# Kernel tuning notes

Measured on AMD Instinct MI355X. Metric: run time of the kernel, lower is better.

Reference implementation:

```python
import jax, jax.numpy as jnp
import numpy as np
from jax import lax

NEG = -1e30  # log-space 'zero' (avoid -inf for numerical safety)
EPS = 1e-7   # keras.backend.epsilon(), added before log in ctc_batch_cost


def _ctc_loss(y_pred, y_true):
    """CTC negative log-likelihood, full input/label lengths, blank = C-1.

    y_pred: [B, T, C] probabilities (post-softmax, as keras ctc_batch_cost expects)
    y_true: [B, L] int labels in [0, C-2]
    returns [B, 1] loss per example (matches keras ctc_batch_cost output shape)
    """
    B, T, C = y_pred.shape
    L = y_true.shape[1]
    S = 2 * L + 1
    blank = C - 1

    logp = jnp.log(y_pred + EPS)  # [B, T, C]

    # Extended label sequence: blank, l1, blank, l2, ..., lL, blank
    ext = jnp.full((B, S), blank, dtype=y_true.dtype)
    ext = ext.at[:, 1::2].set(y_true)  # [B, S]

    # s-2 skip transition allowed iff ext[s] != blank and ext[s] != ext[s-2]
    allow = jnp.concatenate(
        [jnp.zeros((B, 2), dtype=bool),
         (ext[:, 2:] != blank) & (ext[:, 2:] != ext[:, :-2])], axis=1)  # [B, S]

    # Gather log-probs of extended labels per time step: [T, B, S]
    logp_t = jnp.transpose(logp, (1, 0, 2))  # [T, B, C]
    idx = jnp.broadcast_to(ext[None, :, :], (T, B, S))
    lp_ext = jnp.take_along_axis(logp_t, idx, axis=2)  # [T, B, S]

    # alpha init at t=0: only s=0 (blank) and s=1 (first label) reachable
    alpha0 = jnp.full((B, S), NEG, dtype=logp.dtype)
    alpha0 = alpha0.at[:, 0].set(lp_ext[0, :, 0])
    alpha0 = alpha0.at[:, 1].set(lp_ext[0, :, 1])

    neg1 = jnp.full((B, 1), NEG, dtype=logp.dtype)
    neg2 = jnp.full((B, 2), NEG, dtype=logp.dtype)

    def step(alpha, lp):
        a1 = jnp.concatenate([neg1, alpha[:, :-1]], axis=1)
        a2 = jnp.concatenate([neg2, alpha[:, :-2]], axis=1)
        a = jnp.logaddexp(alpha, a1)
        a = jnp.logaddexp(a, jnp.where(allow, a2, NEG))
        return a + lp, None

    alphaT, _ = lax.scan(step, alpha0, lp_ext[1:])  # sequential over T-1 steps

    loss = -jnp.logaddexp(alphaT[:, S - 1], alphaT[:, S - 2])  # [B]
    return loss[:, None]


def setup_inputs() -> dict:
    key = jax.random.key(0)
    k1, k2 = jax.random.split(key)
    B, T, C, L = 512, 512, 128, 64
    logits = jax.random.normal(k1, (B, T, C), dtype=jnp.float32)
    y_pred = jax.nn.softmax(logits, axis=-1)  # ctc_batch_cost expects probabilities
    y_true = jax.random.randint(k2, (B, L), 0, C - 1)  # labels in [0, C-2]; blank=C-1
    return {"y_true": y_true, "y_pred": y_pred}


def reference(y_true, y_pred):
    return _ctc_loss(y_pred, y_true)
```

## Files before the change

kernel.cpp:

```cpp
#include <hip/hip_runtime.h>
#include <hip/hip_bf16.h>


typedef unsigned int u32;
typedef unsigned long long u64;

constexpr int B = 512, T = 512, C = 128, L = 64;
constexpr int NCHUNK = T / 8;
constexpr float EPS = 1e-7f;
constexpr float LN2 = 0.69314718055994530942f;

__device__ __forceinline__ u32 rne16(u32 b) {
    return (b + 0x7FFFu + ((b >> 16) & 1u)) >> 16;
}
__device__ __forceinline__ double dpp64_shr1(double x) {
    union { double d; u32 u[2]; } in, out;
    in.d = x;
    out.u[0] = (u32)__builtin_amdgcn_update_dpp(0, (int)in.u[0], 0x138, 0xF, 0xF, false);
    out.u[1] = (u32)__builtin_amdgcn_update_dpp(0, (int)in.u[1], 0x138, 0xF, 0xF, false);
    return out.d;
}
template <int CTRL>
__device__ __forceinline__ u32 dpp_maxu_step(u32 m) {
    u32 t = (u32)__builtin_amdgcn_update_dpp(0, (int)m, CTRL, 0xF, 0xF, false);
    return m > t ? m : t;
}
__device__ __forceinline__ double exp2_exact(int e) {
    union { double d; u64 u; } s; s.u = (u64)(1023 + e) << 52; return s.d;
}

__global__ __launch_bounds__(512)
void ctc_fused(const int* __restrict__ y_true,
               const float* __restrict__ y_pred,
               float* __restrict__ out) {
    __shared__ uint4 sG[NCHUNK * 65];

    const int b    = blockIdx.x;
    const int wave = threadIdx.x >> 6;
    const int lane = threadIdx.x & 63;

    const int lab  = y_true[b * L + lane];
    const int perm = (lab >> 1) << 2;
    const bool sel_hi = (lab & 1);

    {
        const u64* __restrict__ base =
            (const u64*)(y_pred + (size_t)b * T * C) + lane;
        const int c0 = wave * 8;

        u64 buf[2][8];
#pragma unroll
        for (int j = 0; j < 8; ++j)
            buf[0][j] = __builtin_nontemporal_load(base + (c0 * 8 + j) * 64);

#pragma unroll
        for (int i = 0; i < 8; ++i) {
            const int c = c0 + i;
            if (i + 1 < 8) {
#pragma unroll
                for (int j = 0; j < 8; ++j)
                    buf[(i + 1) & 1][j] =
                        __builtin_nontemporal_load(base + ((c + 1) * 8 + j) * 64);
            }
            const u64* row = buf[i & 1];

            u32 gl[8], gb[8];
#pragma unroll
            for (int j = 0; j < 8; ++j) {
                const int lo = (int)(u32)row[j];
                const int hi = (int)(u32)(row[j] >> 32);
                const int vx = __builtin_amdgcn_ds_bpermute(perm, lo);
                const int vy = __builtin_amdgcn_ds_bpermute(perm, hi);
                gl[j] = __float_as_uint(__int_as_float(sel_hi ? vy : vx) + EPS);
                gb[j] = __float_as_uint(__int_as_float(__shfl(hi, 63)) + EPS);
            }
            u32 wl[4], wb[4];
#pragma unroll
            for (int q = 0; q < 4; ++q) {
                wl[q] = rne16(gl[2 * q]) | (rne16(gl[2 * q + 1]) << 16);
                wb[q] = rne16(gb[2 * q]) | (rne16(gb[2 * q + 1]) << 16);
            }
            sG[c * 65 + lane] = make_uint4(wl[0], wl[1], wl[2], wl[3]);
            if (lane == 0)
                sG[c * 65 + 64] = make_uint4(wb[0], wb[1], wb[2], wb[3]);
        }
    }
    __syncthreads();
    if (threadIdx.x >= 64) return;

    const int lab_prev = __shfl_up(lab, 1);
    const bool allow1 = (lane >= 1) && (lab != lab_prev);

    uint4 so[4], sb[4];
#pragma unroll
    for (int c = 0; c < 4; ++c) {
        so[c] = sG[c * 65 + lane];
        sb[c] = sG[c * 65 + 64];
    }

    double d0 = (lane == 0) ? 1.0 : 0.0;
    double d1 = 0.0;
    double d2 = 0.0;
    int Ce = 0;

#pragma unroll 4
    for (int c = 0; c < NCHUNK; ++c) {
        const int slot = c & 3;
        const uint4 uo = so[slot];
        const uint4 ub = sb[slot];
        const int nc = c + 4;
        if (nc < NCHUNK) {
            so[slot] = sG[nc * 65 + lane];
            sb[slot] = sG[nc * 65 + 64];
        }

        const u32* ow = (const u32*)&uo;
        const u32* bw = (const u32*)&ub;
#pragma unroll
        for (int j = 0; j < 8; ++j) {
            const u32 wo = ow[j >> 1], wb = bw[j >> 1];
            const float fl = __uint_as_float((j & 1) ? (wo & 0xFFFF0000u) : (wo << 16));
            const float fb = __uint_as_float((j & 1) ? (wb & 0xFFFF0000u) : (wb << 16));
            const double Pl = (double)fl, Pb = (double)fb;
            const double p0  = dpp64_shr1(d1);
            const double s01 = d0 + d1;
            const double sel = allow1 ? p0 : 0.0;
            const double nd0 = (d0 + p0) * Pb;
            const double nd2 = (d2 + d1) * Pb;
            const double nd1 = (s01 + sel) * Pl;
            d0 = nd0; d1 = nd1; d2 = nd2;
        }

        if ((c & 3) == 3) {
            u32 h0 = (u32)__double2hiint(d0);
            u32 h1 = (u32)__double2hiint(d1);
            u32 m = h0 > h1 ? h0 : h1;
            m = dpp_maxu_step<0x111>(m);
            m = dpp_maxu_step<0x112>(m);
            m = dpp_maxu_step<0x114>(m);
            m = dpp_maxu_step<0x118>(m);
            m = dpp_maxu_step<0x142>(m);
            m = dpp_maxu_step<0x143>(m);
            const u32 M = (u32)__builtin_amdgcn_readlane((int)m, 63);
            const int e = (int)((M >> 20) & 0x7FFu) - 1023;
            const double s = exp2_exact(-e);
            d0 *= s; d1 *= s; d2 *= s;
            Ce += e;
        }
    }

    if (lane == 63) {
        const double sum = d1 + d2;
        const int ee = ((__double2hiint(sum) >> 20) & 0x7FF) - 1023;
        const float mant = (float)(sum * exp2_exact(-ee));
        out[b] = -((float)(Ce + ee) + __log2f(mant)) * LN2;
    }
}

extern "C" void kernel_launch(void* const* d_in, const int* in_sizes, int n_in,
                              void* d_out, int out_size, void* d_ws, size_t ws_size,
                              hipStream_t stream) {
    const int*   y_true = (const int*)d_in[0];
    const float* y_pred = (const float*)d_in[1];
    float*       out    = (float*)d_out;
    ctc_fused<<<dim3(B), dim3(512), 0, stream>>>(y_true, y_pred, out);
}
```

Measured before the change: 205.1 us.

## Overlap CTC alpha recursion with gather stage using per-chunk LDS ready flags

Replaces the block-wide barrier between the gather/convert stage and the sequential alpha recursion with per-chunk ready flags in shared memory. Waves 1-7 gather chunks 0..55 in interleaved order, and wave 0 gathers the last 8 chunks before starting the recursion. It then spin-waits only on the chunk it needs next, so the serial scan can start while the other waves are still loading. The blank broadcast now uses readlane instead of a shuffle. This adds spin-wait polling and relies on relaxed-store ordering after an explicit LDS wait.

Measured after the change: 200.6 us. 1.02x faster.

```diff
diff --git a/kernel.cpp b/kernel.cpp
--- a/kernel.cpp
+++ b/kernel.cpp
@@ -7,6 +7,7 @@
 
 constexpr int B = 512, T = 512, C = 128, L = 64;
 constexpr int NCHUNK = T / 8;
+constexpr int W0_FIRST = 56;
 constexpr float EPS = 1e-7f;
 constexpr float LN2 = 0.69314718055994530942f;
 
@@ -28,12 +29,17 @@
 __device__ __forceinline__ double exp2_exact(int e) {
     union { double d; u64 u; } s; s.u = (u64)(1023 + e) << 52; return s.d;
 }
+__device__ __forceinline__ void wait_ready(int* f) {
+    while (__hip_atomic_load(f, __ATOMIC_ACQUIRE, __HIP_MEMORY_SCOPE_WORKGROUP) == 0)
+        __builtin_amdgcn_s_sleep(1);
+}
 
 __global__ __launch_bounds__(512)
 void ctc_fused(const int* __restrict__ y_true,
                const float* __restrict__ y_pred,
                float* __restrict__ out) {
     __shared__ uint4 sG[NCHUNK * 65];
+    __shared__ int   ready[NCHUNK];
 
     const int b    = blockIdx.x;
     const int wave = threadIdx.x >> 6;
@@ -43,26 +49,31 @@
     const int perm = (lab >> 1) << 2;
     const bool sel_hi = (lab & 1);
 
+    if (threadIdx.x < NCHUNK) ready[threadIdx.x] = 0;
+    __syncthreads();
+
     {
         const u64* __restrict__ base =
             (const u64*)(y_pred + (size_t)b * T * C) + lane;
-        const int c0 = wave * 8;
+        const int start  = (wave == 0) ? W0_FIRST : (wave - 1);
+        const int stride = (wave == 0) ? 1 : 7;
 
         u64 buf[2][8];
 #pragma unroll
         for (int j = 0; j < 8; ++j)
-            buf[0][j] = __builtin_nontemporal_load(base + (c0 * 8 + j) * 64);
+            buf[0][j] = __builtin_nontemporal_load(base + (start * 8 + j) * 64);
 
 #pragma unroll
-        for (int i = 0; i < 8; ++i) {
-            const int c = c0 + i;
-            if (i + 1 < 8) {
+        for (int k = 0; k < 8; ++k) {
+            const int c = start + stride * k;
+            if (k + 1 < 8) {
+                const int cn = c + stride;
 #pragma unroll
                 for (int j = 0; j < 8; ++j)
-                    buf[(i + 1) & 1][j] =
-                        __builtin_nontemporal_load(base + ((c + 1) * 8 + j) * 64);
+                    buf[(k + 1) & 1][j] =
+                        __builtin_nontemporal_load(base + (cn * 8 + j) * 64);
             }
-            const u64* row = buf[i & 1];
+            const u64* row = buf[k & 1];
 
             u32 gl[8], gb[8];
 #pragma unroll
@@ -72,7 +83,8 @@
                 const int vx = __builtin_amdgcn_ds_bpermute(perm, lo);
                 const int vy = __builtin_amdgcn_ds_bpermute(perm, hi);
                 gl[j] = __float_as_uint(__int_as_float(sel_hi ? vy : vx) + EPS);
-                gb[j] = __float_as_uint(__int_as_float(__shfl(hi, 63)) + EPS);
+                gb[j] = __float_as_uint(
+                    __int_as_float(__builtin_amdgcn_readlane(hi, 63)) + EPS);
             }
             u32 wl[4], wb[4];
 #pragma unroll
@@ -83,10 +95,14 @@
             sG[c * 65 + lane] = make_uint4(wl[0], wl[1], wl[2], wl[3]);
             if (lane == 0)
                 sG[c * 65 + 64] = make_uint4(wb[0], wb[1], wb[2], wb[3]);
+
+            asm volatile("s_waitcnt lgkmcnt(0)" ::: "memory");
+            if (lane == 0)
+                __hip_atomic_store(&ready[c], 1, __ATOMIC_RELAXED,
+                                   __HIP_MEMORY_SCOPE_WORKGROUP);
         }
     }
-    __syncthreads();
-    if (threadIdx.x >= 64) return;
+    if (wave != 0) return;
 
     const int lab_prev = __shfl_up(lab, 1);
     const bool allow1 = (lane >= 1) && (lab != lab_prev);
@@ -94,6 +110,7 @@
     uint4 so[4], sb[4];
 #pragma unroll
     for (int c = 0; c < 4; ++c) {
+        wait_ready(&ready[c]);
         so[c] = sG[c * 65 + lane];
         sb[c] = sG[c * 65 + 64];
     }
@@ -110,6 +127,7 @@
         const uint4 ub = sb[slot];
         const int nc = c + 4;
         if (nc < NCHUNK) {
+            if (nc < W0_FIRST) wait_ready(&ready[nc]);
             so[slot] = sG[nc * 65 + lane];
             sb[slot] = sG[nc * 65 + 64];
         }
```
